# Performance work log

Measured on AMD Instinct MI355X. Metric: run time of the kernel, lower is better.

The kernel has to match this reference:

```python
import jax, jax.numpy as jnp
import numpy as np

NUM_NODES = 102400
NUM_EDGES = 3276800
NUM_GRAPHS = 1024
LAMBDA_MAX = 2.0


def setup_inputs() -> dict:
    key = jax.random.key(0)
    ks = jax.random.split(key, 12)
    inp = {}
    inp['x'] = jax.random.normal(ks[0], (NUM_NODES, 128), dtype=jnp.float32)
    inp['edge_index'] = jax.random.randint(ks[1], (2, NUM_EDGES), 0, NUM_NODES, dtype=jnp.int32).astype(jnp.int64)
    inp['edge_attr'] = jax.random.uniform(ks[2], (NUM_EDGES,), dtype=jnp.float32)
    inp['batch'] = jnp.sort(jax.random.randint(ks[3], (NUM_NODES,), 0, NUM_GRAPHS, dtype=jnp.int32).astype(jnp.int64))
    inp['w1'] = jax.random.normal(ks[4], (3, 128, 64), dtype=jnp.float32) * 0.05
    inp['b1'] = jax.random.normal(ks[5], (64,), dtype=jnp.float32) * 0.05
    inp['w2'] = jax.random.normal(ks[6], (3, 64, 64), dtype=jnp.float32) * 0.05
    inp['b2'] = jax.random.normal(ks[7], (64,), dtype=jnp.float32) * 0.05
    inp['w3'] = jax.random.normal(ks[8], (3, 64, 128), dtype=jnp.float32) * 0.05
    inp['b3'] = jax.random.normal(ks[9], (128,), dtype=jnp.float32) * 0.05
    inp['lin_w'] = jax.random.normal(ks[10], (128, 2), dtype=jnp.float32) * 0.05
    inp['lin_b'] = jax.random.normal(ks[11], (2,), dtype=jnp.float32) * 0.05
    return inp


def _cheb_norm(edge_index, edge_attr, num_nodes):
    # PyG ChebConv.__norm__ with normalization='sym', lambda_max=2.0:
    #   L = I - D^{-1/2} A D^{-1/2};  Lhat = (2/lambda_max) * L - I
    # off-diagonal weights: -(2/lmax) * d_i^{-1/2} w_ij d_j^{-1/2}
    # diagonal coefficient:  (2/lmax) - 1  (== 0 for lmax = 2)
    src, dst = edge_index[0], edge_index[1]
    deg = jax.ops.segment_sum(edge_attr, src, num_segments=num_nodes)
    dinv = jnp.where(deg > 0, jax.lax.rsqrt(jnp.where(deg > 0, deg, 1.0)), 0.0)
    w = -(2.0 / LAMBDA_MAX) * dinv[src] * edge_attr * dinv[dst]
    diag = (2.0 / LAMBDA_MAX) - 1.0
    return w, diag


def _cheb_conv(x, src, dst, norm_w, diag, weight, bias):
    # weight: [K, Fin, Fout]; Chebyshev recurrence T0=x, T1=Lhat x, Tk=2 Lhat T_{k-1} - T_{k-2}
    n = x.shape[0]

    def spmv(v):  # Lhat @ v via edge-list scatter/gather
        return jax.ops.segment_sum(norm_w[:, None] * v[src], dst, num_segments=n) + diag * v

    Tx0 = x
    out = Tx0 @ weight[0]
    Tx1 = spmv(Tx0)
    out = out + Tx1 @ weight[1]
    for k in range(2, weight.shape[0]):
        Tx2 = 2.0 * spmv(Tx1) - Tx0
        out = out + Tx2 @ weight[k]
        Tx0, Tx1 = Tx1, Tx2
    return out + bias


def reference(x, edge_index, edge_attr, batch, w1, b1, w2, b2, w3, b3, lin_w, lin_b):
    n = x.shape[0]
    src, dst = edge_index[0], edge_index[1]
    norm_w, diag = _cheb_norm(edge_index, edge_attr, n)
    h = jax.nn.relu(_cheb_conv(x, src, dst, norm_w, diag, w1, b1))
    h = jax.nn.relu(_cheb_conv(h, src, dst, norm_w, diag, w2, b2))
    h = jax.nn.relu(_cheb_conv(h, src, dst, norm_w, diag, w3, b3))
    # global_mean_pool over graph ids
    sums = jax.ops.segment_sum(h, batch, num_segments=NUM_GRAPHS)
    cnts = jax.ops.segment_sum(jnp.ones((n,), h.dtype), batch, num_segments=NUM_GRAPHS)
    pooled = sums / jnp.maximum(cnts, 1.0)[:, None]
    return pooled @ lin_w + lin_b
```

## Files before the change

### kernel.cpp

```cpp
#include <hip/hip_runtime.h>
#include <cstddef>
#include <cstdint>

#define N_NODES 102400
#define N_EDGES 3276800
#define N_GRAPHS 1024
#define NBUCK 400
#define NBB 512
#define EPB 6400
#define MAXB 12288
#define N64 ((size_t)N_NODES * 64)

typedef unsigned short ushortT;
typedef unsigned int uintT;
typedef __attribute__((ext_vector_type(8))) short bf16x8;
typedef __attribute__((ext_vector_type(4))) float f32x4;

__device__ __forceinline__ float b2f(ushortT h) {
    return __uint_as_float(((uintT)h) << 16);
}
__device__ __forceinline__ ushortT f2b(float f) {
    uintT u = __float_as_uint(f);
    uintT r = (u + 0x7fffu + ((u >> 16) & 1u)) >> 16;
    return (ushortT)r;
}
__device__ __forceinline__ float loF(uintT w) { return __uint_as_float(w << 16); }
__device__ __forceinline__ float hiF(uintT w) { return __uint_as_float(w & 0xffff0000u); }

__global__ __launch_bounds__(256) void k_binA(const int* __restrict__ src,
                                              const int* __restrict__ dst,
                                              int* __restrict__ blkCntD,
                                              int* __restrict__ blkCntS) {
    __shared__ int hd[NBUCK], hs[NBUCK];
    int t = threadIdx.x;
    for (int i = t; i < NBUCK; i += 256) { hd[i] = 0; hs[i] = 0; }
    __syncthreads();
    int base = blockIdx.x * EPB;
    for (int k = 0; k < EPB / 256; k++) {
        int e = base + k * 256 + t;
        atomicAdd(&hd[dst[e] >> 8], 1);
        atomicAdd(&hs[src[e] >> 8], 1);
    }
    __syncthreads();
    for (int i = t; i < NBUCK; i += 256) {
        blkCntD[(size_t)blockIdx.x * NBUCK + i] = hd[i];
        blkCntS[(size_t)blockIdx.x * NBUCK + i] = hs[i];
    }
}

__global__ __launch_bounds__(256) void k_bbase(const int* __restrict__ blkCnt,
                                               int* __restrict__ blkRel,
                                               int* __restrict__ bucketTot) {
    __shared__ int sc[NBB];
    int b = blockIdx.x, t = threadIdx.x;
    int v0 = blkCnt[(size_t)t * NBUCK + b];
    int v1 = blkCnt[(size_t)(t + 256) * NBUCK + b];
    sc[t] = v0; sc[t + 256] = v1;
    __syncthreads();
    for (int o = 1; o < NBB; o <<= 1) {
        int x0 = (t >= o) ? sc[t - o] : 0;
        int x1 = (t + 256 >= o) ? sc[t + 256 - o] : 0;
        __syncthreads();
        sc[t] += x0; sc[t + 256] += x1;
        __syncthreads();
    }
    blkRel[(size_t)t * NBUCK + b] = sc[t] - v0;
    blkRel[(size_t)(t + 256) * NBUCK + b] = sc[t + 256] - v1;
    if (t == 255) bucketTot[b] = sc[NBB - 1];
}

__global__ void k_bscan(const int* __restrict__ bucketTotD,
                        const int* __restrict__ bucketTotS,
                        int* __restrict__ binBaseD,
                        int* __restrict__ binBaseS,
                        int* __restrict__ rowp) {
    int t = threadIdx.x;
    if (t == 0) {
        int run = 0;
        for (int i = 0; i < NBUCK; i++) { binBaseD[i] = run; run += bucketTotD[i]; }
        binBaseD[NBUCK] = run;
        rowp[N_NODES] = run;
    } else if (t == 64) {
        int run = 0;
        for (int i = 0; i < NBUCK; i++) { binBaseS[i] = run; run += bucketTotS[i]; }
        binBaseS[NBUCK] = run;
    }
}

__global__ __launch_bounds__(256) void k_binB(const int* __restrict__ src,
                                              const int* __restrict__ dst,
                                              const float* __restrict__ attr,
                                              const int* __restrict__ blkCnt,
                                              const int* __restrict__ blkRel,
                                              const int* __restrict__ binBaseD,
                                              int2* __restrict__ edsD) {
    __shared__ int spos[EPB];
    __shared__ int sx[EPB];
    __shared__ int sy[EPB];
    __shared__ int lcur[NBUCK];
    __shared__ int delta[NBUCK];
    int bx = blockIdx.x, t = threadIdx.x;

    int* sc = sx;
    int v0 = blkCnt[(size_t)bx * NBUCK + t];
    int v1 = (t + 256 < NBUCK) ? blkCnt[(size_t)bx * NBUCK + t + 256] : 0;
    sc[t] = v0; sc[t + 256] = v1;
    __syncthreads();
    for (int o = 1; o < 512; o <<= 1) {
        int x0 = (t >= o) ? sc[t - o] : 0;
        int x1 = (t + 256 >= o) ? sc[t + 256 - o] : 0;
        __syncthreads();
        sc[t] += x0; sc[t + 256] += x1;
        __syncthreads();
    }
    {
        int e0 = sc[t] - v0;
        lcur[t] = e0;
        delta[t] = binBaseD[t] + blkRel[(size_t)bx * NBUCK + t] - e0;
        if (t + 256 < NBUCK) {
            int e1 = sc[t + 256] - v1;
            lcur[t + 256] = e1;
            delta[t + 256] = binBaseD[t + 256] + blkRel[(size_t)bx * NBUCK + t + 256] - e1;
        }
    }
    __syncthreads();

    int base = bx * EPB;
    for (int k = 0; k < EPB / 256; k++) {
        int e = base + k * 256 + t;
        int s = src[e], d = dst[e];
        int a = __float_as_int(attr[e]);
        int bkt = d >> 8;
        int lp = atomicAdd(&lcur[bkt], 1);
        spos[lp] = lp + delta[bkt];
        sx[lp] = (s << 8) | (d & 255);
        sy[lp] = a;
    }
    __syncthreads();
    for (int k = 0; k < EPB / 256; k++) {
        int i = k * 256 + t;
        edsD[spos[i]] = make_int2(sx[i], sy[i]);
    }
}

__global__ __launch_bounds__(256) void k_binBS(const int* __restrict__ src,
                                               const float* __restrict__ attr,
                                               const int* __restrict__ blkCnt,
                                               const int* __restrict__ blkRel,
                                               const int* __restrict__ binBaseS,
                                               int2* __restrict__ edsS) {
    __shared__ int spos[EPB];
    __shared__ int sx[EPB];
    __shared__ int sy[EPB];
    __shared__ int lcur[NBUCK];
    __shared__ int delta[NBUCK];
    int bx = blockIdx.x, t = threadIdx.x;

    int* sc = sx;
    int v0 = blkCnt[(size_t)bx * NBUCK + t];
    int v1 = (t + 256 < NBUCK) ? blkCnt[(size_t)bx * NBUCK + t + 256] : 0;
    sc[t] = v0; sc[t + 256] = v1;
    __syncthreads();
    for (int o = 1; o < 512; o <<= 1) {
        int x0 = (t >= o) ? sc[t - o] : 0;
        int x1 = (t + 256 >= o) ? sc[t + 256 - o] : 0;
        __syncthreads();
        sc[t] += x0; sc[t + 256] += x1;
        __syncthreads();
    }
    {
        int e0 = sc[t] - v0;
        lcur[t] = e0;
        delta[t] = binBaseS[t] + blkRel[(size_t)bx * NBUCK + t] - e0;
        if (t + 256 < NBUCK) {
            int e1 = sc[t + 256] - v1;
            lcur[t + 256] = e1;
            delta[t + 256] = binBaseS[t + 256] + blkRel[(size_t)bx * NBUCK + t + 256] - e1;
        }
    }
    __syncthreads();

    int base = bx * EPB;
    for (int k = 0; k < EPB / 256; k++) {
        int e = base + k * 256 + t;
        int s = src[e];
        int a = __float_as_int(attr[e]);
        int bkt = s >> 8;
        int lp = atomicAdd(&lcur[bkt], 1);
        spos[lp] = lp + delta[bkt];
        sx[lp] = s & 255;
        sy[lp] = a;
    }
    __syncthreads();
    for (int k = 0; k < EPB / 256; k++) {
        int i = k * 256 + t;
        edsS[spos[i]] = make_int2(sx[i], sy[i]);
    }
}

__global__ __launch_bounds__(256) void k_deg(const int2* __restrict__ edsS,
                                             const int* __restrict__ binBaseS,
                                             float* __restrict__ dinv) {
    __shared__ float degL[256];
    int b = blockIdx.x, t = threadIdx.x;
    degL[t] = 0.f;
    __syncthreads();
    int s0 = binBaseS[b], s1 = binBaseS[b + 1];
    for (int i = s0 + t; i < s1; i += 256) {
        int2 e = edsS[i];
        atomicAdd(&degL[e.x], __int_as_float(e.y));
    }
    __syncthreads();
    float d = degL[t];
    dinv[b * 256 + t] = d > 0.f ? rsqrtf(d) : 0.f;
}

__global__ __launch_bounds__(512) void k_csr(const int2* __restrict__ edsD,
                                             const int* __restrict__ binBaseD,
                                             const float* __restrict__ dinvG,
                                             int* __restrict__ rowp,
                                             int2* __restrict__ cedge) {
    __shared__ int cnt2[256 * 16];
    __shared__ int cntL[256];
    __shared__ float dL[256];
    __shared__ int2 st[MAXB];
    int b = blockIdx.x, t = threadIdx.x;
    for (int i = t; i < 256 * 16; i += 512) cnt2[i] = 0;
    if (t < 256) dL[t] = dinvG[b * 256 + t];
    __syncthreads();
    int s0 = binBaseD[b], s1 = binBaseD[b + 1];
    for (int i = s0 + t; i < s1; i += 512) {
        int2 e = edsD[i];
        atomicAdd(&cnt2[(e.x & 255) * 16 + ((e.x >> 8) >> 13)], 1);
    }
    __syncthreads();
    if (t < 256) {
        int run = 0;
#pragma unroll
        for (int o = 0; o < 16; o++) {
            int c = cnt2[t * 16 + o];
            cnt2[t * 16 + o] = run;
            run += c;
        }
        cntL[t] = run;
    }
    __syncthreads();
    int v = (t < 256) ? cntL[t] : 0;
    for (int o = 1; o < 256; o <<= 1) {
        int x = (t < 256 && t >= o) ? cntL[t - o] : 0;
        __syncthreads();
        if (t < 256) cntL[t] += x;
        __syncthreads();
    }
    if (t < 256) {
        int excl = cntL[t] - v;
        rowp[b * 256 + t] = s0 + excl;
#pragma unroll
        for (int o = 0; o < 16; o++) cnt2[t * 16 + o] += excl;
    }
    __syncthreads();
    for (int i = s0 + t; i < s1; i += 512) {
        int2 e = edsD[i];
        int dl = e.x & 255;
        int sg = e.x >> 8;
        float w = -__int_as_float(e.y) * dinvG[sg] * dL[dl];
        int p = atomicAdd(&cnt2[dl * 16 + (sg >> 13)], 1);
        st[p] = make_int2(sg, __float_as_int(w));
    }
    __syncthreads();
    int n = s1 - s0;
    for (int i = t; i < n; i += 512) cedge[s0 + i] = st[i];
}

__global__ __launch_bounds__(256) void k_cast(const float* __restrict__ x,
                                              ushortT* __restrict__ Xhi,
                                              ushortT* __restrict__ Xlo) {
    int i = blockIdx.x * 256 + threadIdx.x;
    int n = i >> 5;
    int kq = (i & 31) * 4;
    float4 v = ((const float4*)x)[i];
    int s = kq >> 6, kk = kq & 63;
    size_t o = (size_t)s * N64 + (size_t)n * 64 + kk;
    ushort4 h, l;
    h.x = f2b(v.x); l.x = f2b(v.x - b2f(h.x));
    h.y = f2b(v.y); l.y = f2b(v.y - b2f(h.y));
    h.z = f2b(v.z); l.z = f2b(v.z - b2f(h.z));
    h.w = f2b(v.w); l.w = f2b(v.w - b2f(h.w));
    *(ushort4*)(Xhi + o) = h;
    *(ushort4*)(Xlo + o) = l;
}

template <int L>
__global__ void k_wprep(const float* __restrict__ w, ushortT* __restrict__ Wth,
                        ushortT* __restrict__ Wtl) {
    int i = blockIdx.x * 256 + threadIdx.x;
    float v;
    if (L == 1) {
        if (i >= 192 * 128) return;
        int n = i / 128, k = i % 128;
        if (n < 64)       v = w[k * 64 + n] - w[16384 + k * 64 + n];
        else if (n < 128) v = w[8192 + k * 64 + (n - 64)];
        else              v = w[16384 + k * 64 + (n - 128)];
    } else if (L == 2) {
        if (i >= 192 * 64) return;
        int n = i / 64, k = i % 64;
        if (n < 64)       v = w[k * 64 + n] - w[8192 + k * 64 + n];
        else if (n < 128) v = w[4096 + k * 64 + (n - 64)];
        else              v = w[8192 + k * 64 + (n - 128)];
    } else {
        if (i >= 128 * 192) return;
        int n = i / 192, k = i % 192;
        v = w[(k >> 6) * 8192 + (k & 63) * 128 + n];
    }
    ushortT h = f2b(v);
    Wth[i] = h;
    Wtl[i] = f2b(v - b2f(h));
}

template <int KTOT, int NTOT, int MODE>
__global__ __launch_bounds__(512) void k_mgemm(
    const ushortT* __restrict__ Ah0, const ushortT* __restrict__ Ah1,
    const ushortT* __restrict__ Ah2, const ushortT* __restrict__ Al0,
    const ushortT* __restrict__ Al1, const ushortT* __restrict__ Al2,
    const ushortT* __restrict__ Wth, const ushortT* __restrict__ Wtl,
    const float* __restrict__ bias, float* __restrict__ outf,
    ushortT* __restrict__ outb) {
    constexpr int KPAD = 72;
    constexpr int NCT = NTOT / 16;
    __shared__ ushortT Bh[NTOT * KPAD];
    __shared__ ushortT Bl[NTOT * KPAD];
    const ushortT* Ah[3] = {Ah0, Ah1, Ah2};
    const ushortT* Al[3] = {Al0, Al1, Al2};
    int t = threadIdx.x;
    int lane = t & 63;
    int wv = t >> 6;
    int m = lane & 15, q = lane >> 4;
    int r0 = blockIdx.x * 256 + wv * 32;
    int ar0 = r0 + m;
    int ar1 = r0 + 16 + m;

    f32x4 acc[2][NCT];
#pragma unroll
    for (int rf = 0; rf < 2; rf++)
#pragma unroll
        for (int ct = 0; ct < NCT; ct++)
#pragma unroll
            for (int j = 0; j < 4; j++) acc[rf][ct][j] = 0.f;

#pragma unroll
    for (int kc = 0; kc < KTOT / 64; kc++) {
        __syncthreads();
        for (int i = t; i < NTOT * 8; i += 512) {
            int col = i >> 3, k = (i & 7) * 8;
            *(uint4*)(Bh + col * KPAD + k) =
                *(const uint4*)(Wth + (size_t)col * KTOT + kc * 64 + k);
            *(uint4*)(Bl + col * KPAD + k) =
                *(const uint4*)(Wtl + (size_t)col * KTOT + kc * 64 + k);
        }
        __syncthreads();
        const ushortT* Ahc = Ah[kc];
        const ushortT* Alc = Al[kc];
#pragma unroll
        for (int ks2 = 0; ks2 < 2; ks2++) {
            int kk = ks2 * 32 + q * 8;
            bf16x8 ah0 = *(const bf16x8*)(Ahc + (size_t)ar0 * 64 + kk);
            bf16x8 al0 = *(const bf16x8*)(Alc + (size_t)ar0 * 64 + kk);
            bf16x8 ah1 = *(const bf16x8*)(Ahc + (size_t)ar1 * 64 + kk);
            bf16x8 al1 = *(const bf16x8*)(Alc + (size_t)ar1 * 64 + kk);
#pragma unroll
            for (int ct = 0; ct < NCT; ct++) {
                int bo = (ct * 16 + m) * KPAD + ks2 * 32 + q * 8;
                bf16x8 bh = *(const bf16x8*)(Bh + bo);
                bf16x8 bl = *(const bf16x8*)(Bl + bo);
                acc[0][ct] = __builtin_amdgcn_mfma_f32_16x16x32_bf16(ah0, bh, acc[0][ct], 0, 0, 0);
                acc[0][ct] = __builtin_amdgcn_mfma_f32_16x16x32_bf16(al0, bh, acc[0][ct], 0, 0, 0);
                acc[0][ct] = __builtin_amdgcn_mfma_f32_16x16x32_bf16(ah0, bl, acc[0][ct], 0, 0, 0);
                acc[1][ct] = __builtin_amdgcn_mfma_f32_16x16x32_bf16(ah1, bh, acc[1][ct], 0, 0, 0);
                acc[1][ct] = __builtin_amdgcn_mfma_f32_16x16x32_bf16(al1, bh, acc[1][ct], 0, 0, 0);
                acc[1][ct] = __builtin_amdgcn_mfma_f32_16x16x32_bf16(ah1, bl, acc[1][ct], 0, 0, 0);
            }
        }
    }

#pragma unroll
    for (int rf = 0; rf < 2; rf++)
#pragma unroll
        for (int ct = 0; ct < NCT; ct++)
#pragma unroll
            for (int rg = 0; rg < 4; rg++) {
                int row = r0 + rf * 16 + q * 4 + rg;
                float v = acc[rf][ct][rg];
                if (MODE == 0) {
                    if (ct < 8)
                        outf[(size_t)row * 128 + ct * 16 + m] = v;
                    else
                        outb[(size_t)row * 64 + (ct - 8) * 16 + m] = f2b(v);
                } else {
                    int col = ct * 16 + m;
                    outf[(size_t)row * 128 + col] = fmaxf(v + bias[col], 0.f);
                }
            }
}

template <int MODE, int SA, bool AUXB, bool WLO>
__global__ __launch_bounds__(256) void k_spmm(const int* __restrict__ rowp,
                                              const int2* __restrict__ cedge,
                                              const ushortT* __restrict__ Xb,
                                              const float* __restrict__ auxF,
                                              const ushortT* __restrict__ auxH,
                                              const ushortT* __restrict__ auxL,
                                              const float* __restrict__ bias,
                                              ushortT* __restrict__ Yh,
                                              ushortT* __restrict__ Yl) {
    int node = blockIdx.x * 4 + (threadIdx.x >> 6);
    int lane = threadIdx.x & 63;
    int q = lane >> 3;
    int f = (lane & 7) * 8;
    int s = rowp[node], e = rowp[node + 1];
    const ushortT* Xf = Xb + f;
    float a0 = 0.f, a1 = 0.f, a2 = 0.f, a3 = 0.f;
    float a4 = 0.f, a5 = 0.f, a6 = 0.f, a7 = 0.f;
    for (int i = s; i < e; i += 16) {
        int i0 = min(i + q, e - 1);
        int i1 = min(i + 8 + q, e - 1);
        int2 ed0 = cedge[i0];
        int2 ed1 = cedge[i1];
        float w0 = (i + q < e) ? __int_as_float(ed0.y) : 0.f;
        float w1 = (i + 8 + q < e) ? __int_as_float(ed1.y) : 0.f;
        uint4 u0 = *(const uint4*)(Xf + ((size_t)ed0.x << 6));
        uint4 u1 = *(const uint4*)(Xf + ((size_t)ed1.x << 6));
        a0 = fmaf(w0, loF(u0.x), a0);
        a1 = fmaf(w0, hiF(u0.x), a1);
        a2 = fmaf(w0, loF(u0.y), a2);
        a3 = fmaf(w0, hiF(u0.y), a3);
        a4 = fmaf(w0, loF(u0.z), a4);
        a5 = fmaf(w0, hiF(u0.z), a5);
        a6 = fmaf(w0, loF(u0.w), a6);
        a7 = fmaf(w0, hiF(u0.w), a7);
        a0 = fmaf(w1, loF(u1.x), a0);
        a1 = fmaf(w1, hiF(u1.x), a1);
        a2 = fmaf(w1, loF(u1.y), a2);
        a3 = fmaf(w1, hiF(u1.y), a3);
        a4 = fmaf(w1, loF(u1.z), a4);
        a5 = fmaf(w1, hiF(u1.z), a5);
        a6 = fmaf(w1, loF(u1.w), a6);
        a7 = fmaf(w1, hiF(u1.w), a7);
    }
    a0 += __shfl_xor(a0, 8); a0 += __shfl_xor(a0, 16); a0 += __shfl_xor(a0, 32);
    a1 += __shfl_xor(a1, 8); a1 += __shfl_xor(a1, 16); a1 += __shfl_xor(a1, 32);
    a2 += __shfl_xor(a2, 8); a2 += __shfl_xor(a2, 16); a2 += __shfl_xor(a2, 32);
    a3 += __shfl_xor(a3, 8); a3 += __shfl_xor(a3, 16); a3 += __shfl_xor(a3, 32);
    a4 += __shfl_xor(a4, 8); a4 += __shfl_xor(a4, 16); a4 += __shfl_xor(a4, 32);
    a5 += __shfl_xor(a5, 8); a5 += __shfl_xor(a5, 16); a5 += __shfl_xor(a5, 32);
    a6 += __shfl_xor(a6, 8); a6 += __shfl_xor(a6, 16); a6 += __shfl_xor(a6, 32);
    a7 += __shfl_xor(a7, 8); a7 += __shfl_xor(a7, 16); a7 += __shfl_xor(a7, 32);

    if (q == 0 || (WLO && q == 1)) {
        float x0 = 0.f, x1 = 0.f, x2 = 0.f, x3 = 0.f;
        float x4 = 0.f, x5 = 0.f, x6 = 0.f, x7 = 0.f;
        if (MODE != 0) {
            if (AUXB) {
                uint4 ha = *(const uint4*)(auxH + (size_t)node * 64 + f);
                uint4 la = *(const uint4*)(auxL + (size_t)node * 64 + f);
                x0 = loF(ha.x) + loF(la.x);
                x1 = hiF(ha.x) + hiF(la.x);
                x2 = loF(ha.y) + loF(la.y);
                x3 = hiF(ha.y) + hiF(la.y);
                x4 = loF(ha.z) + loF(la.z);
                x5 = hiF(ha.z) + hiF(la.z);
                x6 = loF(ha.w) + loF(la.w);
                x7 = hiF(ha.w) + hiF(la.w);
            } else {
                float4 av0 = *(const float4*)(auxF + (size_t)node * SA + f);
                float4 av1 = *(const float4*)(auxF + (size_t)node * SA + f + 4);
                x0 = av0.x; x1 = av0.y; x2 = av0.z; x3 = av0.w;
                x4 = av1.x; x5 = av1.y; x6 = av1.z; x7 = av1.w;
            }
        }
        float r0, r1, r2, r3, r4, r5, r6, r7;
        if (MODE == 0) {
            r0 = a0; r1 = a1; r2 = a2; r3 = a3;
            r4 = a4; r5 = a5; r6 = a6; r7 = a7;
        } else if (MODE == 1) {
            r0 = x0 + 2.f * a0; r1 = x1 + 2.f * a1;
            r2 = x2 + 2.f * a2; r3 = x3 + 2.f * a3;
            r4 = x4 + 2.f * a4; r5 = x5 + 2.f * a5;
            r6 = x6 + 2.f * a6; r7 = x7 + 2.f * a7;
        } else if (MODE == 2) {
            r0 = 2.f * a0 - x0; r1 = 2.f * a1 - x1;
            r2 = 2.f * a2 - x2; r3 = 2.f * a3 - x3;
            r4 = 2.f * a4 - x4; r5 = 2.f * a5 - x5;
            r6 = 2.f * a6 - x6; r7 = 2.f * a7 - x7;
        } else {
            float4 bv0 = *(const float4*)(bias + f);
            float4 bv1 = *(const float4*)(bias + f + 4);
            r0 = fmaxf(x0 + a0 + bv0.x, 0.f);
            r1 = fmaxf(x1 + a1 + bv0.y, 0.f);
            r2 = fmaxf(x2 + a2 + bv0.z, 0.f);
            r3 = fmaxf(x3 + a3 + bv0.w, 0.f);
            r4 = fmaxf(x4 + a4 + bv1.x, 0.f);
            r5 = fmaxf(x5 + a5 + bv1.y, 0.f);
            r6 = fmaxf(x6 + a6 + bv1.z, 0.f);
            r7 = fmaxf(x7 + a7 + bv1.w, 0.f);
        }
        ushortT h0 = f2b(r0), h1 = f2b(r1), h2 = f2b(r2), h3 = f2b(r3);
        ushortT h4 = f2b(r4), h5 = f2b(r5), h6 = f2b(r6), h7 = f2b(r7);
        if (q == 0) {
            uint4 pk;
            pk.x = (uintT)h0 | ((uintT)h1 << 16);
            pk.y = (uintT)h2 | ((uintT)h3 << 16);
            pk.z = (uintT)h4 | ((uintT)h5 << 16);
            pk.w = (uintT)h6 | ((uintT)h7 << 16);
            *(uint4*)(Yh + (size_t)node * 64 + f) = pk;
        } else {
            uint4 pk;
            pk.x = (uintT)f2b(r0 - b2f(h0)) | ((uintT)f2b(r1 - b2f(h1)) << 16);
            pk.y = (uintT)f2b(r2 - b2f(h2)) | ((uintT)f2b(r3 - b2f(h3)) << 16);
            pk.z = (uintT)f2b(r4 - b2f(h4)) | ((uintT)f2b(r5 - b2f(h5)) << 16);
            pk.w = (uintT)f2b(r6 - b2f(h6)) | ((uintT)f2b(r7 - b2f(h7)) << 16);
            *(uint4*)(Yl + (size_t)node * 64 + f) = pk;
        }
    }
}

__global__ __launch_bounds__(128) void k_pool(const int* __restrict__ batch,
                                              const float* __restrict__ H3,
                                              float* __restrict__ pooled,
                                              float* __restrict__ gcnt) {
    int t = threadIdx.x;
    int n0 = blockIdx.x * 64;
    int g = batch[n0];
    float a = 0.f;
    int c = 0;
    for (int k = 0; k < 64; k++) {
        int gn = batch[n0 + k];
        if (gn != g) {
            atomicAdd(&pooled[(size_t)g * 128 + t], a);
            if (t == 0) atomicAdd(&gcnt[g], (float)c);
            g = gn; a = 0.f; c = 0;
        }
        a += H3[(size_t)(n0 + k) * 128 + t];
        c++;
    }
    atomicAdd(&pooled[(size_t)g * 128 + t], a);
    if (t == 0) atomicAdd(&gcnt[g], (float)c);
}

__global__ void k_final(const float* __restrict__ pooled, const float* __restrict__ gcnt,
                        const float* __restrict__ lin_w, const float* __restrict__ lin_b,
                        float* __restrict__ out) {
    int g = blockIdx.x * 4 + (threadIdx.x >> 6);
    int lane = threadIdx.x & 63;
    if (g >= N_GRAPHS) return;
    float inv = 1.f / fmaxf(gcnt[g], 1.f);
    float v0 = pooled[(size_t)g * 128 + lane] * inv;
    float v1 = pooled[(size_t)g * 128 + 64 + lane] * inv;
    float p0 = v0 * lin_w[lane * 2 + 0] + v1 * lin_w[(lane + 64) * 2 + 0];
    float p1 = v0 * lin_w[lane * 2 + 1] + v1 * lin_w[(lane + 64) * 2 + 1];
    for (int o = 32; o > 0; o >>= 1) {
        p0 += __shfl_down(p0, o);
        p1 += __shfl_down(p1, o);
    }
    if (lane == 0) {
        out[g * 2 + 0] = p0 + lin_b[0];
        out[g * 2 + 1] = p1 + lin_b[1];
    }
}

extern "C" void kernel_launch(void* const* d_in, const int* in_sizes, int n_in,
                              void* d_out, int out_size, void* d_ws, size_t ws_size,
                              hipStream_t stream) {
    const float* x     = (const float*)d_in[0];
    const int*   src   = (const int*)d_in[1];
    const int*   dst   = src + N_EDGES;
    const float* eattr = (const float*)d_in[2];
    const int*   batch = (const int*)d_in[3];
    const float* w1    = (const float*)d_in[4];
    const float* b1    = (const float*)d_in[5];
    const float* w2    = (const float*)d_in[6];
    const float* b2    = (const float*)d_in[7];
    const float* w3    = (const float*)d_in[8];
    const float* b3    = (const float*)d_in[9];
    const float* lin_w = (const float*)d_in[10];
    const float* lin_b = (const float*)d_in[11];
    float* out = (float*)d_out;

    char* ws = (char*)d_ws;
    size_t off = 0;
    auto alloc = [&](size_t bytes) -> char* {
        char* p = ws + off;
        off += (bytes + 255) & ~(size_t)255;
        return p;
    };
    int*   blkCntD   = (int*)  alloc((size_t)NBB * NBUCK * 4);
    int*   blkCntS   = (int*)  alloc((size_t)NBB * NBUCK * 4);
    int*   blkRelD   = (int*)  alloc((size_t)NBB * NBUCK * 4);
    int*   blkRelS   = (int*)  alloc((size_t)NBB * NBUCK * 4);
    int*   bucketTotD = (int*) alloc(NBUCK * 4);
    int*   bucketTotS = (int*) alloc(NBUCK * 4);
    int*   binBaseD  = (int*)  alloc((NBUCK + 1) * 4);
    int*   binBaseS  = (int*)  alloc((NBUCK + 1) * 4);
    float* dinv      = (float*)alloc((size_t)N_NODES * 4);
    int*   rowp      = (int*)  alloc((size_t)(N_NODES + 1) * 4);
    ushortT* Wt1h   = (ushortT*)alloc(192 * 128 * 2);
    ushortT* Wt1l   = (ushortT*)alloc(192 * 128 * 2);
    ushortT* Wt2h   = (ushortT*)alloc(192 * 64 * 2);
    ushortT* Wt2l   = (ushortT*)alloc(192 * 64 * 2);
    ushortT* Wt3h   = (ushortT*)alloc(128 * 192 * 2);
    ushortT* Wt3l   = (ushortT*)alloc(128 * 192 * 2);
    float* pooled   = (float*)alloc((size_t)(N_GRAPHS * 128 + N_GRAPHS) * 4);
    float* gcnt     = pooled + (size_t)N_GRAPHS * 128;
    int2*  cedge    = (int2*) alloc((size_t)N_EDGES * 8);
    char*  Buf1     = alloc((size_t)N_EDGES * 16);
    char*  Buf2     = alloc((size_t)N_NODES * 128 * 4);
    char*  Buf3     = alloc(4 * N64 * 2);

    int2* edsD = (int2*)Buf1;
    int2* edsS = edsD + N_EDGES;
    ushortT* Xhi  = (ushortT*)Buf1;
    ushortT* Xlo  = Xhi + 2 * N64;
    ushortT* GThi = (ushortT*)Buf1;
    float* P  = (float*)Buf2;
    float* H3 = (float*)Buf2;
    ushortT* G0    = (ushortT*)Buf3;
    ushortT* Qhi   = G0 + N64;
    ushortT* H1hi  = G0 + 2 * N64;
    ushortT* H1lo  = G0 + 3 * N64;
    ushortT* GTlo0 = G0;
    ushortT* GTlo1 = H1hi;
    ushortT* GTlo2 = H1lo;

    hipMemsetAsync(pooled, 0, (size_t)(N_GRAPHS * 128 + N_GRAPHS) * 4, stream);

    k_binA<<<NBB, 256, 0, stream>>>(src, dst, blkCntD, blkCntS);
    k_bbase<<<NBUCK, 256, 0, stream>>>(blkCntD, blkRelD, bucketTotD);
    k_bbase<<<NBUCK, 256, 0, stream>>>(blkCntS, blkRelS, bucketTotS);
    k_bscan<<<1, 128, 0, stream>>>(bucketTotD, bucketTotS, binBaseD, binBaseS, rowp);
    k_binBS<<<NBB, 256, 0, stream>>>(src, eattr, blkCntS, blkRelS, binBaseS, edsS);
    k_deg<<<NBUCK, 256, 0, stream>>>(edsS, binBaseS, dinv);
    k_binB<<<NBB, 256, 0, stream>>>(src, dst, eattr, blkCntD, blkRelD, binBaseD, edsD);
    k_csr<<<NBUCK, 512, 0, stream>>>(edsD, binBaseD, dinv, rowp, cedge);

    k_cast<<<N_NODES * 32 / 256, 256, 0, stream>>>(x, Xhi, Xlo);
    k_wprep<1><<<96, 256, 0, stream>>>(w1, Wt1h, Wt1l);
    k_wprep<2><<<48, 256, 0, stream>>>(w2, Wt2h, Wt2l);
    k_wprep<3><<<96, 256, 0, stream>>>(w3, Wt3h, Wt3l);

    k_mgemm<128, 192, 0><<<N_NODES / 256, 512, 0, stream>>>(
        Xhi, Xhi + N64, nullptr, Xlo, Xlo + N64, nullptr, Wt1h, Wt1l, nullptr, P, G0);
    k_spmm<1, 128, false, false><<<N_NODES / 4, 256, 0, stream>>>(
        rowp, cedge, G0, P + 64, nullptr, nullptr, nullptr, Qhi, nullptr);
    k_spmm<3, 128, false, true><<<N_NODES / 4, 256, 0, stream>>>(
        rowp, cedge, Qhi, P, nullptr, nullptr, b1, H1hi, H1lo);

    k_mgemm<64, 192, 0><<<N_NODES / 256, 512, 0, stream>>>(
        H1hi, nullptr, nullptr, H1lo, nullptr, nullptr, Wt2h, Wt2l, nullptr, P, G0);
    k_spmm<1, 128, false, false><<<N_NODES / 4, 256, 0, stream>>>(
        rowp, cedge, G0, P + 64, nullptr, nullptr, nullptr, Qhi, nullptr);
    k_spmm<3, 128, false, true><<<N_NODES / 4, 256, 0, stream>>>(
        rowp, cedge, Qhi, P, nullptr, nullptr, b2, GThi, GTlo0);

    k_spmm<0, 64, false, true><<<N_NODES / 4, 256, 0, stream>>>(
        rowp, cedge, GThi, nullptr, nullptr, nullptr, nullptr, GThi + N64, GTlo1);
    k_spmm<2, 64, true, true><<<N_NODES / 4, 256, 0, stream>>>(
        rowp, cedge, GThi + N64, nullptr, GThi, GTlo0, nullptr, GThi + 2 * N64, GTlo2);
    k_mgemm<192, 128, 1><<<N_NODES / 256, 512, 0, stream>>>(
        GThi, GThi + N64, GThi + 2 * N64, GTlo0, GTlo1, GTlo2, Wt3h, Wt3l, b3, H3, nullptr);

    k_pool<<<N_NODES / 64, 128, 0, stream>>>(batch, H3, pooled, gcnt);
    k_final<<<N_GRAPHS / 4, 256, 0, stream>>>(pooled, gcnt, lin_w, lin_b, out);
}
```

Before: 759.6 us.

## Fuse src and dst edge binning into one kernel and vectorize histogram loads

```diff
diff --git a/kernel.cpp b/kernel.cpp
--- a/kernel.cpp
+++ b/kernel.cpp
@@ -36,10 +36,19 @@
     for (int i = t; i < NBUCK; i += 256) { hd[i] = 0; hs[i] = 0; }
     __syncthreads();
     int base = blockIdx.x * EPB;
-    for (int k = 0; k < EPB / 256; k++) {
-        int e = base + k * 256 + t;
-        atomicAdd(&hd[dst[e] >> 8], 1);
-        atomicAdd(&hs[src[e] >> 8], 1);
+    const int4* s4 = (const int4*)(src + base);
+    const int4* d4 = (const int4*)(dst + base);
+    for (int v = t; v < EPB / 4; v += 256) {
+        int4 d = d4[v];
+        int4 s = s4[v];
+        atomicAdd(&hd[d.x >> 8], 1);
+        atomicAdd(&hd[d.y >> 8], 1);
+        atomicAdd(&hd[d.z >> 8], 1);
+        atomicAdd(&hd[d.w >> 8], 1);
+        atomicAdd(&hs[s.x >> 8], 1);
+        atomicAdd(&hs[s.y >> 8], 1);
+        atomicAdd(&hs[s.z >> 8], 1);
+        atomicAdd(&hs[s.w >> 8], 1);
     }
     __syncthreads();
     for (int i = t; i < NBUCK; i += 256) {
@@ -87,114 +96,76 @@
     }
 }
 
-__global__ __launch_bounds__(256) void k_binB(const int* __restrict__ src,
-                                              const int* __restrict__ dst,
-                                              const float* __restrict__ attr,
-                                              const int* __restrict__ blkCnt,
-                                              const int* __restrict__ blkRel,
-                                              const int* __restrict__ binBaseD,
-                                              int2* __restrict__ edsD) {
-    __shared__ int spos[EPB];
-    __shared__ int sx[EPB];
-    __shared__ int sy[EPB];
-    __shared__ int lcur[NBUCK];
-    __shared__ int delta[NBUCK];
+__global__ __launch_bounds__(512) void k_binB2(const int* __restrict__ src,
+                                               const int* __restrict__ dst,
+                                               const float* __restrict__ attr,
+                                               const int* __restrict__ blkCntD,
+                                               const int* __restrict__ blkCntS,
+                                               const int* __restrict__ blkRelD,
+                                               const int* __restrict__ blkRelS,
+                                               const int* __restrict__ binBaseD,
+                                               const int* __restrict__ binBaseS,
+                                               int2* __restrict__ edsD,
+                                               int2* __restrict__ edsS) {
+    __shared__ int sxD[EPB];
+    __shared__ int syD[EPB];
+    __shared__ ushortT spD[EPB];
+    __shared__ int sxS[EPB];
+    __shared__ int syS[EPB];
+    __shared__ ushortT spS[EPB];
+    __shared__ int lcurD[NBUCK], deltaD[NBUCK];
+    __shared__ int lcurS[NBUCK], deltaS[NBUCK];
     int bx = blockIdx.x, t = threadIdx.x;
 
-    int* sc = sx;
-    int v0 = blkCnt[(size_t)bx * NBUCK + t];
-    int v1 = (t + 256 < NBUCK) ? blkCnt[(size_t)bx * NBUCK + t + 256] : 0;
-    sc[t] = v0; sc[t + 256] = v1;
+    int vD = (t < NBUCK) ? blkCntD[(size_t)bx * NBUCK + t] : 0;
+    int vS = (t < NBUCK) ? blkCntS[(size_t)bx * NBUCK + t] : 0;
+    sxD[t] = vD; sxS[t] = vS;
     __syncthreads();
     for (int o = 1; o < 512; o <<= 1) {
-        int x0 = (t >= o) ? sc[t - o] : 0;
-        int x1 = (t + 256 >= o) ? sc[t + 256 - o] : 0;
-        __syncthreads();
-        sc[t] += x0; sc[t + 256] += x1;
-        __syncthreads();
-    }
-    {
-        int e0 = sc[t] - v0;
-        lcur[t] = e0;
-        delta[t] = binBaseD[t] + blkRel[(size_t)bx * NBUCK + t] - e0;
-        if (t + 256 < NBUCK) {
-            int e1 = sc[t + 256] - v1;
-            lcur[t + 256] = e1;
-            delta[t + 256] = binBaseD[t + 256] + blkRel[(size_t)bx * NBUCK + t + 256] - e1;
-        }
+        int xD = (t >= o) ? sxD[t - o] : 0;
+        int xS = (t >= o) ? sxS[t - o] : 0;
+        __syncthreads();
+        sxD[t] += xD; sxS[t] += xS;
+        __syncthreads();
+    }
+    if (t < NBUCK) {
+        int eD = sxD[t] - vD;
+        lcurD[t] = eD;
+        deltaD[t] = binBaseD[t] + blkRelD[(size_t)bx * NBUCK + t] - eD;
+        int eS = sxS[t] - vS;
+        lcurS[t] = eS;
+        deltaS[t] = binBaseS[t] + blkRelS[(size_t)bx * NBUCK + t] - eS;
     }
     __syncthreads();
 
     int base = bx * EPB;
-    for (int k = 0; k < EPB / 256; k++) {
-        int e = base + k * 256 + t;
-        int s = src[e], d = dst[e];
-        int a = __float_as_int(attr[e]);
-        int bkt = d >> 8;
-        int lp = atomicAdd(&lcur[bkt], 1);
-        spos[lp] = lp + delta[bkt];
-        sx[lp] = (s << 8) | (d & 255);
-        sy[lp] = a;
-    }
-    __syncthreads();
-    for (int k = 0; k < EPB / 256; k++) {
-        int i = k * 256 + t;
-        edsD[spos[i]] = make_int2(sx[i], sy[i]);
-    }
-}
-
-__global__ __launch_bounds__(256) void k_binBS(const int* __restrict__ src,
-                                               const float* __restrict__ attr,
-                                               const int* __restrict__ blkCnt,
-                                               const int* __restrict__ blkRel,
-                                               const int* __restrict__ binBaseS,
-                                               int2* __restrict__ edsS) {
-    __shared__ int spos[EPB];
-    __shared__ int sx[EPB];
-    __shared__ int sy[EPB];
-    __shared__ int lcur[NBUCK];
-    __shared__ int delta[NBUCK];
-    int bx = blockIdx.x, t = threadIdx.x;
-
-    int* sc = sx;
-    int v0 = blkCnt[(size_t)bx * NBUCK + t];
-    int v1 = (t + 256 < NBUCK) ? blkCnt[(size_t)bx * NBUCK + t + 256] : 0;
-    sc[t] = v0; sc[t + 256] = v1;
-    __syncthreads();
-    for (int o = 1; o < 512; o <<= 1) {
-        int x0 = (t >= o) ? sc[t - o] : 0;
-        int x1 = (t + 256 >= o) ? sc[t + 256 - o] : 0;
-        __syncthreads();
-        sc[t] += x0; sc[t + 256] += x1;
-        __syncthreads();
-    }
-    {
-        int e0 = sc[t] - v0;
-        lcur[t] = e0;
-        delta[t] = binBaseS[t] + blkRel[(size_t)bx * NBUCK + t] - e0;
-        if (t + 256 < NBUCK) {
-            int e1 = sc[t + 256] - v1;
-            lcur[t + 256] = e1;
-            delta[t + 256] = binBaseS[t + 256] + blkRel[(size_t)bx * NBUCK + t + 256] - e1;
-        }
-    }
-    __syncthreads();
-
-    int base = bx * EPB;
-    for (int k = 0; k < EPB / 256; k++) {
-        int e = base + k * 256 + t;
-        int s = src[e];
-        int a = __float_as_int(attr[e]);
-        int bkt = s >> 8;
-        int lp = atomicAdd(&lcur[bkt], 1);
-        spos[lp] = lp + delta[bkt];
-        sx[lp] = s & 255;
-        sy[lp] = a;
-    }
-    __syncthreads();
-    for (int k = 0; k < EPB / 256; k++) {
-        int i = k * 256 + t;
-        edsS[spos[i]] = make_int2(sx[i], sy[i]);
+    for (int v = t; v < EPB / 2; v += 512) {
+        int e0 = base + v * 2;
+        int2 s2 = *(const int2*)(src + e0);
+        int2 d2 = *(const int2*)(dst + e0);
+        float2 a2 = *(const float2*)(attr + e0);
+        int bkt, lp;
+        bkt = d2.x >> 8;
+        lp = atomicAdd(&lcurD[bkt], 1);
+        spD[lp] = (ushortT)bkt; sxD[lp] = (s2.x << 8) | (d2.x & 255);
+        syD[lp] = __float_as_int(a2.x);
+        bkt = s2.x >> 8;
+        lp = atomicAdd(&lcurS[bkt], 1);
+        spS[lp] = (ushortT)bkt; sxS[lp] = s2.x & 255;
+        syS[lp] = __float_as_int(a2.x);
+        bkt = d2.y >> 8;
+        lp = atomicAdd(&lcurD[bkt], 1);
+        spD[lp] = (ushortT)bkt; sxD[lp] = (s2.y << 8) | (d2.y & 255);
+        syD[lp] = __float_as_int(a2.y);
+        bkt = s2.y >> 8;
+        lp = atomicAdd(&lcurS[bkt], 1);
+        spS[lp] = (ushortT)bkt; sxS[lp] = s2.y & 255;
+        syS[lp] = __float_as_int(a2.y);
+    }
+    __syncthreads();
+    for (int i = t; i < EPB; i += 512) {
+        edsD[i + deltaD[spD[i]]] = make_int2(sxD[i], syD[i]);
+        edsS[i + deltaS[spS[i]]] = make_int2(sxS[i], syS[i]);
     }
 }
 
@@ -636,9 +607,10 @@
     k_bbase<<<NBUCK, 256, 0, stream>>>(blkCntD, blkRelD, bucketTotD);
     k_bbase<<<NBUCK, 256, 0, stream>>>(blkCntS, blkRelS, bucketTotS);
     k_bscan<<<1, 128, 0, stream>>>(bucketTotD, bucketTotS, binBaseD, binBaseS, rowp);
-    k_binBS<<<NBB, 256, 0, stream>>>(src, eattr, blkCntS, blkRelS, binBaseS, edsS);
+    k_binB2<<<NBB, 512, 0, stream>>>(src, dst, eattr, blkCntD, blkCntS,
+                                     blkRelD, blkRelS, binBaseD, binBaseS,
+                                     edsD, edsS);
     k_deg<<<NBUCK, 256, 0, stream>>>(edsS, binBaseS, dinv);
-    k_binB<<<NBB, 256, 0, stream>>>(src, dst, eattr, blkCntD, blkRelD, binBaseD, edsD);
     k_csr<<<NBUCK, 512, 0, stream>>>(edsD, binBaseD, dinv, rowp, cedge);
 
     k_cast<<<N_NODES * 32 / 256, 256, 0, stream>>>(x, Xhi, Xlo);
```

Result: faster. 739.1 us (-2.7%).
